# Optimization experiments

Hardware: AMD Instinct MI355X
Metric: run time of the kernel (lower is better)

Reference implementation:

```python
import jax, jax.numpy as jnp
import numpy as np

NUM_EXPERT = 32
IN_FEAT = 256
OUT_FEAT = 256
TOTAL_TOKENS = 524288
CAPACITY = 16896  # static per-expert pad, > max expected count


def setup_inputs() -> dict:
    key = jax.random.key(0)
    k_inp, k_w = jax.random.split(key)
    inp = jax.random.normal(k_inp, (TOTAL_TOKENS, IN_FEAT), dtype=jnp.float32)
    # weight initialized like nn.Linear (kaiming-uniform-ish); scale of randn is fine for a numeric baseline
    weight = jax.random.normal(k_w, (NUM_EXPERT, OUT_FEAT, IN_FEAT), dtype=jnp.float32) * (1.0 / np.sqrt(IN_FEAT))
    # variable-sized expert groups summing exactly to TOTAL_TOKENS (tokens assumed pre-sorted by expert)
    rng = np.random.default_rng(0)
    counts = rng.multinomial(TOTAL_TOKENS, np.ones(NUM_EXPERT) / NUM_EXPERT)
    assert counts.max() <= CAPACITY and counts.sum() == TOTAL_TOKENS
    fwd_expert_count = jnp.asarray(counts, dtype=jnp.int64)
    return {"inp": inp, "weight": weight, "fwd_expert_count": fwd_expert_count, "capacity": CAPACITY}


def reference(inp, weight, fwd_expert_count, capacity):
    # Grouped GEMM: for expert e, out[seg_e] = inp[seg_e] @ weight[e].T
    E = weight.shape[0]
    T = inp.shape[0]
    counts = fwd_expert_count.astype(jnp.int32)
    cum = jnp.cumsum(counts)                       # [E] inclusive prefix sums
    starts = cum - counts                          # [E] segment starts
    tok = jnp.arange(T, dtype=jnp.int32)
    eid = jnp.searchsorted(cum, tok, side='right') # [T] expert id per token
    pos = tok - starts[eid]                        # [T] slot within expert group
    # Scatter tokens into padded per-expert buffer [E, capacity, in]
    buf = jnp.zeros((E, capacity, inp.shape[1]), dtype=inp.dtype).at[eid, pos].set(inp)
    # Batched matmul against per-expert weights [E, out, in] -> [E, capacity, out]
    y = jnp.einsum('eci,eoi->eco', buf, weight)
    # Gather back to token order [T, out]
    return y[eid, pos]
```

## Files before the change

kernel.cpp:

```cpp
#include <hip/hip_runtime.h>
#include <cstdint>
#include <cstddef>

#define NEXPERT 32
#define KIN 256
#define NOUT 256
#define NTOK 524288
#define BM 64

typedef float f32x4 __attribute__((ext_vector_type(4)));
typedef __bf16 bf16x8 __attribute__((ext_vector_type(8)));
typedef unsigned short u16;
typedef u16 u16x8 __attribute__((ext_vector_type(8)));

union BF8 { u16x8 u; bf16x8 b; };

__device__ __forceinline__ u16 f2bf(float f) {
  unsigned u = __float_as_uint(f);
  return (u16)((u + 0x7FFFu + ((u >> 16) & 1u)) >> 16);
}

__global__ void conv_w_kernel(const float* __restrict__ w, u16* __restrict__ wb) {
  const int i = (blockIdx.x * 256 + threadIdx.x) * 4;
  const float4 v = *reinterpret_cast<const float4*>(w + i);
  ushort4 o;
  o.x = f2bf(v.x); o.y = f2bf(v.y); o.z = f2bf(v.z); o.w = f2bf(v.w);
  *reinterpret_cast<ushort4*>(wb + i) = o;
}

template<bool WSBF>
__global__ __launch_bounds__(256, 3)
void moe_gemm_kernel(const float* __restrict__ inp,
                     const float* __restrict__ w32,
                     const u16* __restrict__ wbf,
                     const int* __restrict__ counts,
                     float* __restrict__ out)
{
  __shared__ u16 sA[BM * 64];
  __shared__ int sCum[NEXPERT + 1];

  const int tid  = threadIdx.x;
  const int lane = tid & 63;
  const int wv   = tid >> 6;
  const int l15  = lane & 15;
  const int lg   = lane >> 4;

  if (tid == 0) {
    const long long* c64 = reinterpret_cast<const long long*>(counts);
    const long long probe = c64[0];
    const bool is64 = (probe >= 0 && probe < (1ll << 31));
    int c = 0;
    sCum[0] = 0;
    for (int i2 = 0; i2 < NEXPERT; ++i2) {
      const int ci = is64 ? (int)c64[i2] : counts[i2];
      c += ci;
      sCum[i2 + 1] = c;
    }
  }
  __syncthreads();

  const int t0 = blockIdx.x * BM;
  const int t1 = t0 + BM;

  int ee = 0;
  while (sCum[ee + 1] <= t0) ++ee;

  int rb = t0;
  while (rb < t1) {
    const int re = min(t1, sCum[ee + 1]);
    if (re > rb) {
      const int e = ee;
      f32x4 acc[4][4];
      const f32x4 zero = {0.f, 0.f, 0.f, 0.f};
#pragma unroll
      for (int m = 0; m < 4; ++m)
#pragma unroll
        for (int n = 0; n < 4; ++n)
          acc[m][n] = zero;

      for (int ks = 0; ks < 4; ++ks) {
        const int k0 = ks * 64;
        __syncthreads();
        {
          const int srow = tid >> 2;
          const int cst  = (tid & 3) << 4;
          const float4* sp4 =
              reinterpret_cast<const float4*>(inp + (size_t)(t0 + srow) * KIN + (k0 + cst));
          const float4 v0 = sp4[0], v1 = sp4[1], v2 = sp4[2], v3 = sp4[3];
          u16x8 h0, h1;
          h0[0]=f2bf(v0.x); h0[1]=f2bf(v0.y); h0[2]=f2bf(v0.z); h0[3]=f2bf(v0.w);
          h0[4]=f2bf(v1.x); h0[5]=f2bf(v1.y); h0[6]=f2bf(v1.z); h0[7]=f2bf(v1.w);
          h1[0]=f2bf(v2.x); h1[1]=f2bf(v2.y); h1[2]=f2bf(v2.z); h1[3]=f2bf(v2.w);
          h1[4]=f2bf(v3.x); h1[5]=f2bf(v3.y); h1[6]=f2bf(v3.z); h1[7]=f2bf(v3.w);
          const int rx = (srow & 7) << 4;
          char* rbase = reinterpret_cast<char*>(sA) + srow * 128;
          const int cb = cst << 1;
          *reinterpret_cast<u16x8*>(rbase + ((cb     ) ^ rx)) = h0;
          *reinterpret_cast<u16x8*>(rbase + ((cb + 16) ^ rx)) = h1;
        }
        BF8 bfr[4][2];
        if (WSBF) {
          const u16* wb = wbf + ((size_t)e << 16);
#pragma unroll
          for (int n = 0; n < 4; ++n) {
            const int rown = (wv << 6) + (n << 4) + l15;
#pragma unroll
            for (int kk = 0; kk < 2; ++kk)
              bfr[n][kk].u = *reinterpret_cast<const u16x8*>(
                  wb + (size_t)rown * KIN + k0 + kk * 32 + lg * 8);
          }
        } else {
          const float* wf = w32 + ((size_t)e << 16);
#pragma unroll
          for (int n = 0; n < 4; ++n) {
            const int rown = (wv << 6) + (n << 4) + l15;
#pragma unroll
            for (int kk = 0; kk < 2; ++kk) {
              const float4* p = reinterpret_cast<const float4*>(
                  wf + (size_t)rown * KIN + k0 + kk * 32 + lg * 8);
              const float4 a0 = p[0], a1 = p[1];
              u16x8 h;
              h[0]=f2bf(a0.x); h[1]=f2bf(a0.y); h[2]=f2bf(a0.z); h[3]=f2bf(a0.w);
              h[4]=f2bf(a1.x); h[5]=f2bf(a1.y); h[6]=f2bf(a1.z); h[7]=f2bf(a1.w);
              bfr[n][kk].u = h;
            }
          }
        }
        __syncthreads();
#pragma unroll
        for (int kk = 0; kk < 2; ++kk) {
          BF8 afr[4];
#pragma unroll
          for (int m = 0; m < 4; ++m) {
            const int row = (m << 4) + l15;
            const int kb  = kk * 64 + (lg << 4);
            afr[m].u = *reinterpret_cast<const u16x8*>(
                reinterpret_cast<const char*>(sA) + row * 128 + (kb ^ ((row & 7) << 4)));
          }
#pragma unroll
          for (int m = 0; m < 4; ++m)
#pragma unroll
            for (int n = 0; n < 4; ++n)
              acc[m][n] = __builtin_amdgcn_mfma_f32_16x16x32_bf16(
                  afr[m].b, bfr[n][kk].b, acc[m][n], 0, 0, 0);
        }
      }
#pragma unroll
      for (int m = 0; m < 4; ++m) {
        const int rbase = t0 + (m << 4) + (lg << 2);
#pragma unroll
        for (int n = 0; n < 4; ++n) {
          float* op = out + (size_t)rbase * NOUT + (wv << 6) + (n << 4) + l15;
#pragma unroll
          for (int j = 0; j < 4; ++j) {
            const int rg = rbase + j;
            if (rg >= rb && rg < re)
              op[(size_t)j * NOUT] = acc[m][n][j];
          }
        }
      }
    }
    rb = re > rb ? re : rb;
    ++ee;
  }
}

extern "C" void kernel_launch(void* const* d_in, const int* in_sizes, int n_in,
                              void* d_out, int out_size, void* d_ws, size_t ws_size,
                              hipStream_t stream) {
  const float* inp    = (const float*)d_in[0];
  const float* w      = (const float*)d_in[1];
  const int*   counts = (const int*)d_in[2];
  float*       out    = (float*)d_out;

  const size_t wbytes = (size_t)NEXPERT * NOUT * KIN * 2;
  const bool usews = (ws_size >= wbytes);

  if (usews) {
    u16* wbf = (u16*)d_ws;
    const int total = NEXPERT * NOUT * KIN;
    conv_w_kernel<<<total / (256 * 4), 256, 0, stream>>>(w, wbf);
    moe_gemm_kernel<true><<<NTOK / BM, 256, 0, stream>>>(inp, w, wbf, counts, out);
  } else {
    moe_gemm_kernel<false><<<NTOK / BM, 256, 0, stream>>>(inp, w, nullptr, counts, out);
  }
}
```

Baseline: 273.4 us.

## Double-buffer A tile in LDS and software-pipeline global loads with MFMA compute

Splits the A staging buffer into two LDS buffers and unrolls the four K-steps so the global loads and bf16 conversion of the next slice overlap MFMA compute on the current one. It also computes the expert prefix sum with a wavefront scan and finds the expert with a ballot, and it adds an unguarded store path for tiles that belong to a single expert. The launch-bounds occupancy hint is dropped. These changes target load latency and the per-row bounds checks, at the cost of more registers and LDS, which may reduce occupancy.

```diff
diff --git a/kernel.cpp b/kernel.cpp
--- a/kernel.cpp
+++ b/kernel.cpp
@@ -28,15 +28,72 @@
   *reinterpret_cast<ushort4*>(wb + i) = o;
 }
 
+__device__ __forceinline__ void gload(const float4* ap4, int ks, float4 (&v)[4]) {
+#pragma unroll
+  for (int i = 0; i < 4; ++i) v[i] = ap4[ks * 16 + i];
+}
+
+__device__ __forceinline__ void cvtw(const float4 (&v)[4], char* rbase, int cb, int rx) {
+  u16x8 h0, h1;
+  h0[0]=f2bf(v[0].x); h0[1]=f2bf(v[0].y); h0[2]=f2bf(v[0].z); h0[3]=f2bf(v[0].w);
+  h0[4]=f2bf(v[1].x); h0[5]=f2bf(v[1].y); h0[6]=f2bf(v[1].z); h0[7]=f2bf(v[1].w);
+  h1[0]=f2bf(v[2].x); h1[1]=f2bf(v[2].y); h1[2]=f2bf(v[2].z); h1[3]=f2bf(v[2].w);
+  h1[4]=f2bf(v[3].x); h1[5]=f2bf(v[3].y); h1[6]=f2bf(v[3].z); h1[7]=f2bf(v[3].w);
+  *reinterpret_cast<u16x8*>(rbase + ((cb     ) ^ rx)) = h0;
+  *reinterpret_cast<u16x8*>(rbase + ((cb + 16) ^ rx)) = h1;
+}
+
 template<bool WSBF>
-__global__ __launch_bounds__(256, 3)
+__device__ __forceinline__ void ldb(const u16* wB, const float* wF, int ks, BF8 (&dst)[4][2]) {
+  if (WSBF) {
+#pragma unroll
+    for (int n = 0; n < 4; ++n)
+#pragma unroll
+      for (int kk = 0; kk < 2; ++kk)
+        dst[n][kk].u = *reinterpret_cast<const u16x8*>(wB + n * (16 * KIN) + ks * 64 + kk * 32);
+  } else {
+#pragma unroll
+    for (int n = 0; n < 4; ++n)
+#pragma unroll
+      for (int kk = 0; kk < 2; ++kk) {
+        const float4* p = reinterpret_cast<const float4*>(wF + n * (16 * KIN) + ks * 64 + kk * 32);
+        const float4 x = p[0], y = p[1];
+        u16x8 h;
+        h[0]=f2bf(x.x); h[1]=f2bf(x.y); h[2]=f2bf(x.z); h[3]=f2bf(x.w);
+        h[4]=f2bf(y.x); h[5]=f2bf(y.y); h[6]=f2bf(y.z); h[7]=f2bf(y.w);
+        dst[n][kk].u = h;
+      }
+  }
+}
+
+__device__ __forceinline__ void compute(const char* abase, int lg, int arx,
+                                        const BF8 (&bfr)[4][2], f32x4 (&acc)[4][4]) {
+#pragma unroll
+  for (int kk = 0; kk < 2; ++kk) {
+    BF8 af[4];
+#pragma unroll
+    for (int m = 0; m < 4; ++m)
+      af[m].u = *reinterpret_cast<const u16x8*>(
+          abase + m * 2048 + ((kk * 64 + (lg << 4)) ^ arx));
+#pragma unroll
+    for (int m = 0; m < 4; ++m)
+#pragma unroll
+      for (int n = 0; n < 4; ++n)
+        acc[m][n] = __builtin_amdgcn_mfma_f32_16x16x32_bf16(
+            af[m].b, bfr[n][kk].b, acc[m][n], 0, 0, 0);
+  }
+}
+
+template<bool WSBF>
+__global__ __launch_bounds__(256)
 void moe_gemm_kernel(const float* __restrict__ inp,
                      const float* __restrict__ w32,
                      const u16* __restrict__ wbf,
                      const int* __restrict__ counts,
                      float* __restrict__ out)
 {
-  __shared__ u16 sA[BM * 64];
+  __shared__ u16 sA0[BM * 64];
+  __shared__ u16 sA1[BM * 64];
   __shared__ int sCum[NEXPERT + 1];
 
   const int tid  = threadIdx.x;
@@ -45,123 +102,110 @@
   const int l15  = lane & 15;
   const int lg   = lane >> 4;
 
-  if (tid == 0) {
+  if (tid < 32) {
     const long long* c64 = reinterpret_cast<const long long*>(counts);
-    const long long probe = c64[0];
-    const bool is64 = (probe >= 0 && probe < (1ll << 31));
-    int c = 0;
-    sCum[0] = 0;
-    for (int i2 = 0; i2 < NEXPERT; ++i2) {
-      const int ci = is64 ? (int)c64[i2] : counts[i2];
-      c += ci;
-      sCum[i2 + 1] = c;
+    const long long p0 = c64[0];
+    const bool is64 = (p0 >= 0 && p0 < (1ll << 31));
+    int c = is64 ? (int)c64[tid] : counts[tid];
+#pragma unroll
+    for (int d = 1; d < 32; d <<= 1) {
+      int o = __shfl_up(c, d, 64);
+      if (tid >= d) c += o;
     }
+    sCum[tid + 1] = c;
+    if (tid == 0) sCum[0] = 0;
   }
   __syncthreads();
 
   const int t0 = blockIdx.x * BM;
   const int t1 = t0 + BM;
 
-  int ee = 0;
-  while (sCum[ee + 1] <= t0) ++ee;
+  int ee;
+  {
+    const int v = (lane < NEXPERT) ? sCum[lane + 1] : 0x7fffffff;
+    const unsigned long long m = __ballot(v <= t0);
+    ee = __popcll(m);
+  }
+
+  const int srow = tid >> 2;
+  const int scol = (tid & 3) << 4;
+  const float4* ap4 =
+      reinterpret_cast<const float4*>(inp + (size_t)(t0 + srow) * KIN + scol);
+  char* const r0 = reinterpret_cast<char*>(sA0) + srow * 128;
+  char* const r1 = reinterpret_cast<char*>(sA1) + srow * 128;
+  const int rx = (srow & 7) << 4;
+  const int cb = scol << 1;
+  const int arx = (l15 & 7) << 4;
+  const char* const a0 = reinterpret_cast<const char*>(sA0) + l15 * 128;
+  const char* const a1 = reinterpret_cast<const char*>(sA1) + l15 * 128;
 
   int rb = t0;
+  int e = ee;
   while (rb < t1) {
-    const int re = min(t1, sCum[ee + 1]);
+    const int re = min(t1, sCum[e + 1]);
     if (re > rb) {
-      const int e = ee;
+      const size_t wro = ((size_t)e << 16) + (size_t)((wv << 6) + l15) * KIN + lg * 8;
+      const u16*   wB  = wbf + wro;
+      const float* wF  = w32 + wro;
+
       f32x4 acc[4][4];
       const f32x4 zero = {0.f, 0.f, 0.f, 0.f};
 #pragma unroll
       for (int m = 0; m < 4; ++m)
 #pragma unroll
-        for (int n = 0; n < 4; ++n)
-          acc[m][n] = zero;
-
-      for (int ks = 0; ks < 4; ++ks) {
-        const int k0 = ks * 64;
-        __syncthreads();
-        {
-          const int srow = tid >> 2;
-          const int cst  = (tid & 3) << 4;
-          const float4* sp4 =
-              reinterpret_cast<const float4*>(inp + (size_t)(t0 + srow) * KIN + (k0 + cst));
-          const float4 v0 = sp4[0], v1 = sp4[1], v2 = sp4[2], v3 = sp4[3];
-          u16x8 h0, h1;
-          h0[0]=f2bf(v0.x); h0[1]=f2bf(v0.y); h0[2]=f2bf(v0.z); h0[3]=f2bf(v0.w);
-          h0[4]=f2bf(v1.x); h0[5]=f2bf(v1.y); h0[6]=f2bf(v1.z); h0[7]=f2bf(v1.w);
-          h1[0]=f2bf(v2.x); h1[1]=f2bf(v2.y); h1[2]=f2bf(v2.z); h1[3]=f2bf(v2.w);
-          h1[4]=f2bf(v3.x); h1[5]=f2bf(v3.y); h1[6]=f2bf(v3.z); h1[7]=f2bf(v3.w);
-          const int rx = (srow & 7) << 4;
-          char* rbase = reinterpret_cast<char*>(sA) + srow * 128;
-          const int cb = cst << 1;
-          *reinterpret_cast<u16x8*>(rbase + ((cb     ) ^ rx)) = h0;
-          *reinterpret_cast<u16x8*>(rbase + ((cb + 16) ^ rx)) = h1;
-        }
-        BF8 bfr[4][2];
-        if (WSBF) {
-          const u16* wb = wbf + ((size_t)e << 16);
+        for (int n = 0; n < 4; ++n) acc[m][n] = zero;
+
+      float4 va[4], vb[4];
+      BF8 bA[4][2], bB[4][2];
+
+      gload(ap4, 0, va);
+      gload(ap4, 1, vb);
+      ldb<WSBF>(wB, wF, 0, bA);
+      __syncthreads();
+      cvtw(va, r0, cb, rx);
+      __syncthreads();
+
+      ldb<WSBF>(wB, wF, 1, bB); cvtw(vb, r1, cb, rx); gload(ap4, 2, va);
+      compute(a0, lg, arx, bA, acc);
+      __syncthreads();
+      ldb<WSBF>(wB, wF, 2, bA); cvtw(va, r0, cb, rx); gload(ap4, 3, vb);
+      compute(a1, lg, arx, bB, acc);
+      __syncthreads();
+      ldb<WSBF>(wB, wF, 3, bB); cvtw(vb, r1, cb, rx);
+      compute(a0, lg, arx, bA, acc);
+      __syncthreads();
+      compute(a1, lg, arx, bB, acc);
+
+      const bool full = (rb == t0) & (re == t1);
+      if (full) {
+#pragma unroll
+        for (int m = 0; m < 4; ++m) {
+          const int rbase = t0 + (m << 4) + (lg << 2);
 #pragma unroll
           for (int n = 0; n < 4; ++n) {
-            const int rown = (wv << 6) + (n << 4) + l15;
-#pragma unroll
-            for (int kk = 0; kk < 2; ++kk)
-              bfr[n][kk].u = *reinterpret_cast<const u16x8*>(
-                  wb + (size_t)rown * KIN + k0 + kk * 32 + lg * 8);
-          }
-        } else {
-          const float* wf = w32 + ((size_t)e << 16);
-#pragma unroll
-          for (int n = 0; n < 4; ++n) {
-            const int rown = (wv << 6) + (n << 4) + l15;
-#pragma unroll
-            for (int kk = 0; kk < 2; ++kk) {
-              const float4* p = reinterpret_cast<const float4*>(
-                  wf + (size_t)rown * KIN + k0 + kk * 32 + lg * 8);
-              const float4 a0 = p[0], a1 = p[1];
-              u16x8 h;
-              h[0]=f2bf(a0.x); h[1]=f2bf(a0.y); h[2]=f2bf(a0.z); h[3]=f2bf(a0.w);
-              h[4]=f2bf(a1.x); h[5]=f2bf(a1.y); h[6]=f2bf(a1.z); h[7]=f2bf(a1.w);
-              bfr[n][kk].u = h;
-            }
+            float* op = out + (size_t)rbase * NOUT + (wv << 6) + (n << 4) + l15;
+#pragma unroll
+            for (int j = 0; j < 4; ++j) op[(size_t)j * NOUT] = acc[m][n][j];
           }
         }
-        __syncthreads();
-#pragma unroll
-        for (int kk = 0; kk < 2; ++kk) {
-          BF8 afr[4];
-#pragma unroll
-          for (int m = 0; m < 4; ++m) {
-            const int row = (m << 4) + l15;
-            const int kb  = kk * 64 + (lg << 4);
-            afr[m].u = *reinterpret_cast<const u16x8*>(
-                reinterpret_cast<const char*>(sA) + row * 128 + (kb ^ ((row & 7) << 4)));
-          }
-#pragma unroll
-          for (int m = 0; m < 4; ++m)
-#pragma unroll
-            for (int n = 0; n < 4; ++n)
-              acc[m][n] = __builtin_amdgcn_mfma_f32_16x16x32_bf16(
-                  afr[m].b, bfr[n][kk].b, acc[m][n], 0, 0, 0);
-        }
-      }
-#pragma unroll
-      for (int m = 0; m < 4; ++m) {
-        const int rbase = t0 + (m << 4) + (lg << 2);
-#pragma unroll
-        for (int n = 0; n < 4; ++n) {
-          float* op = out + (size_t)rbase * NOUT + (wv << 6) + (n << 4) + l15;
-#pragma unroll
-          for (int j = 0; j < 4; ++j) {
-            const int rg = rbase + j;
-            if (rg >= rb && rg < re)
-              op[(size_t)j * NOUT] = acc[m][n][j];
+      } else {
+#pragma unroll
+        for (int m = 0; m < 4; ++m) {
+          const int rbase = t0 + (m << 4) + (lg << 2);
+#pragma unroll
+          for (int n = 0; n < 4; ++n) {
+            float* op = out + (size_t)rbase * NOUT + (wv << 6) + (n << 4) + l15;
+#pragma unroll
+            for (int j = 0; j < 4; ++j) {
+              const int rg = rbase + j;
+              if (rg >= rb && rg < re) op[(size_t)j * NOUT] = acc[m][n][j];
+            }
           }
         }
       }
     }
     rb = re > rb ? re : rb;
-    ++ee;
+    ++e;
   }
 }
 
```

Result: no change. 272.7 us (-0.3%).
